# Performance work log

Measured on AMD Instinct MI355X. Metric: run time of the kernel, lower is better.

Reference implementation:

```python
import jax, jax.numpy as jnp
import numpy as np

V, BLOCK, L, H, E, B, T = 1024, 2048, 4, 8, 512, 4, 2048
D = E // H  # head dim = 64

def setup_inputs() -> dict:
    key = jax.random.key(0)
    ks = jax.random.split(key, 8)
    s = 0.02
    return {
        "idx": jax.random.randint(ks[0], (B, T), 0, V),
        "wte": jax.random.normal(ks[1], (V, E), jnp.float32) * s,
        "wpe": jax.random.normal(ks[2], (BLOCK, E), jnp.float32) * s,
        "ln1_w": jnp.ones((L, E), jnp.float32),
        "ln1_b": jnp.zeros((L, E), jnp.float32),
        "attn_w": jax.random.normal(ks[3], (L, 3 * E, E), jnp.float32) * s,
        "attn_b": jnp.zeros((L, 3 * E), jnp.float32),
        "proj_w": jax.random.normal(ks[4], (L, E, E), jnp.float32) * s,
        "proj_b": jnp.zeros((L, E), jnp.float32),
        "ln2_w": jnp.ones((L, E), jnp.float32),
        "ln2_b": jnp.zeros((L, E), jnp.float32),
        "fc_w": jax.random.normal(ks[5], (L, 4 * E, E), jnp.float32) * s,
        "fc_b": jnp.zeros((L, 4 * E), jnp.float32),
        "fc2_w": jax.random.normal(ks[6], (L, E, 4 * E), jnp.float32) * s,
        "fc2_b": jnp.zeros((L, E), jnp.float32),
        "lnf_w": jnp.ones((E,), jnp.float32),
        "lnf_b": jnp.zeros((E,), jnp.float32),
    }

def layer_norm(x, w, b, eps=1e-5):
    mu = jnp.mean(x, axis=-1, keepdims=True)
    var = jnp.var(x, axis=-1, keepdims=True)
    return (x - mu) * jax.lax.rsqrt(var + eps) * w + b

def reference(idx, wte, wpe, ln1_w, ln1_b, attn_w, attn_b, proj_w, proj_b,
              ln2_w, ln2_b, fc_w, fc_b, fc2_w, fc2_b, lnf_w, lnf_b):
    b, t = idx.shape
    x = wte[idx] + wpe[:t]  # (B,T,E)
    causal = jnp.tril(jnp.ones((t, t), bool))
    scale = 1.0 / np.sqrt(D)

    def block(x, p):
        l1w, l1b, aw, ab, pw, pb, l2w, l2b, fw, fb, f2w, f2b = p
        h = layer_norm(x, l1w, l1b)
        qkv = h @ aw.T + ab  # (B,T,3E)
        q, k, v = jnp.split(qkv, 3, axis=-1)
        q = q.reshape(b, t, H, D)
        k = k.reshape(b, t, H, D)
        v = v.reshape(b, t, H, D)
        att = jnp.einsum('bqhd,bkhd->bhqk', q, k) * scale
        att = jnp.where(causal, att, -jnp.inf)
        att = jax.nn.softmax(att, axis=-1)
        y = jnp.einsum('bhqk,bkhd->bqhd', att, v).reshape(b, t, E)
        x = x + y @ pw.T + pb
        h2 = layer_norm(x, l2w, l2b)
        h2 = jax.nn.gelu(h2 @ fw.T + fb, approximate=False)
        x = x + h2 @ f2w.T + f2b
        return x, None

    params = (ln1_w, ln1_b, attn_w, attn_b, proj_w, proj_b,
              ln2_w, ln2_b, fc_w, fc_b, fc2_w, fc2_b)
    x, _ = jax.lax.scan(block, x, params)
    x = layer_norm(x, lnf_w, lnf_b)
    logits = x @ wte.T  # tied lm_head
    return logits
```

## Files before the change

kernel.cpp:

```cpp
#include <hip/hip_runtime.h>
#include <hip/hip_bf16.h>
#include <math.h>

#define B_ 4
#define T_ 2048
#define E_ 512
#define H_ 8
#define D_ 64
#define L_ 4
#define V_ 1024
#define NROWS (B_*T_)
#define KBLK 64
#define KVPAD 72
#define PPAD 72
#define SPLT 16

typedef __hip_bfloat16 bf16;
typedef __attribute__((ext_vector_type(8))) short bf16x8;
typedef __attribute__((ext_vector_type(4))) float f32x4;

__device__ __forceinline__ short f2bf_s(float f) {
    union { bf16 h; short s; } t; t.h = __float2bfloat16(f); return t.s;
}

__device__ __forceinline__ void gload_lds16(const bf16* g, bf16* l) {
    __builtin_amdgcn_global_load_lds((const __attribute__((address_space(1))) void*)g,
                                     (__attribute__((address_space(3))) void*)l, 16, 0, 0);
}

__global__ void f2bf_all(const float* __restrict__ s0, const float* __restrict__ s1,
                         const float* __restrict__ s2, const float* __restrict__ s3,
                         const float* __restrict__ s4, bf16* __restrict__ dst) {
    size_t gi = (size_t)blockIdx.x * 1024 + threadIdx.x * 4;
    const float* src; size_t off;
    if (blockIdx.x < 3072)       { src = s0; off = gi; }
    else if (blockIdx.x < 4096)  { src = s1; off = gi - (size_t)3072 * 1024; }
    else if (blockIdx.x < 8192)  { src = s2; off = gi - (size_t)4096 * 1024; }
    else if (blockIdx.x < 12288) { src = s3; off = gi - (size_t)8192 * 1024; }
    else                         { src = s4; off = gi - (size_t)12288 * 1024; }
    float4 v = *(const float4*)(src + off);
    union { bf16 h[4]; uint2 u; } t;
    t.h[0] = __float2bfloat16(v.x); t.h[1] = __float2bfloat16(v.y);
    t.h[2] = __float2bfloat16(v.z); t.h[3] = __float2bfloat16(v.w);
    *(uint2*)(dst + gi) = t.u;
}

__global__ void embed_kernel(const int* __restrict__ idx, const float* __restrict__ wte,
                             const float* __restrict__ wpe, float* __restrict__ x) {
    int i = (blockIdx.x * blockDim.x + threadIdx.x) * 4;
    int row = i >> 9;
    int e = i & (E_ - 1);
    int t = row & (T_ - 1);
    int id = idx[row];
    float4 a = *(const float4*)(wte + (size_t)id * E_ + e);
    float4 p = *(const float4*)(wpe + (size_t)t * E_ + e);
    a.x += p.x; a.y += p.y; a.z += p.z; a.w += p.w;
    *(float4*)(x + i) = a;
}

__global__ __launch_bounds__(512) void layernorm_kernel(const float* __restrict__ x,
                                 const float* __restrict__ w, const float* __restrict__ b,
                                 bf16* __restrict__ out) {
    int wid = threadIdx.x >> 6, lane = threadIdx.x & 63;
    int row = blockIdx.x * 8 + wid;
    const float* xr = x + (size_t)row * E_ + lane * 8;
    float4 a0 = *(const float4*)xr;
    float4 a1 = *(const float4*)(xr + 4);
    float s = (a0.x + a0.y) + (a0.z + a0.w) + (a1.x + a1.y) + (a1.z + a1.w);
    float q = a0.x*a0.x + a0.y*a0.y + a0.z*a0.z + a0.w*a0.w
            + a1.x*a1.x + a1.y*a1.y + a1.z*a1.z + a1.w*a1.w;
    #pragma unroll
    for (int st = 1; st < 64; st <<= 1) { s += __shfl_xor(s, st); q += __shfl_xor(q, st); }
    float mean = s * (1.0f / E_);
    float var = q * (1.0f / E_) - mean * mean;
    float rstd = rsqrtf(var + 1e-5f);
    float4 w0 = *(const float4*)(w + lane * 8), w1 = *(const float4*)(w + lane * 8 + 4);
    float4 b0 = *(const float4*)(b + lane * 8), b1 = *(const float4*)(b + lane * 8 + 4);
    union { bf16 h[8]; uint4 u; } o;
    o.h[0] = __float2bfloat16((a0.x - mean) * rstd * w0.x + b0.x);
    o.h[1] = __float2bfloat16((a0.y - mean) * rstd * w0.y + b0.y);
    o.h[2] = __float2bfloat16((a0.z - mean) * rstd * w0.z + b0.z);
    o.h[3] = __float2bfloat16((a0.w - mean) * rstd * w0.w + b0.w);
    o.h[4] = __float2bfloat16((a1.x - mean) * rstd * w1.x + b1.x);
    o.h[5] = __float2bfloat16((a1.y - mean) * rstd * w1.y + b1.y);
    o.h[6] = __float2bfloat16((a1.z - mean) * rstd * w1.z + b1.z);
    o.h[7] = __float2bfloat16((a1.w - mean) * rstd * w1.w + b1.w);
    *(uint4*)(out + (size_t)row * E_ + lane * 8) = o.u;
}

template<int ACT, int OMODE, bool BIAS, bool QKV>
__global__ __launch_bounds__(256) void gemm_mfma(const bf16* __restrict__ A, const bf16* __restrict__ W,
        const float* __restrict__ bias, float* __restrict__ Cf, bf16* __restrict__ Cb,
        bf16* __restrict__ Vt, int M, int N, int K) {
    __shared__ __align__(16) bf16 As[128][32];
    __shared__ __align__(16) bf16 Bs[128][32];
    int tid = threadIdx.x;
    int lane = tid & 63, wid = tid >> 6;
    int wm = (wid >> 1) * 64, wn = (wid & 1) * 64;
    int m0 = blockIdx.y * 128, n0 = blockIdx.x * 128;

    int srow = wid * 32 + (lane >> 2);
    int scol = (lane & 3) * 8;
    const bf16* ga = A + (size_t)(m0 + srow) * K + scol;
    const bf16* gb = W + (size_t)(n0 + srow) * K + scol;
    int fr = lane & 15, fk = (lane >> 4) * 8;

    f32x4 acc[4][4];
    #pragma unroll
    for (int i = 0; i < 4; ++i)
        #pragma unroll
        for (int j = 0; j < 4; ++j) acc[i][j] = (f32x4){0.f, 0.f, 0.f, 0.f};

    for (int k0 = 0; k0 < K; k0 += 32) {
        gload_lds16(ga,          &As[wid * 32][0]);
        gload_lds16(ga + 16 * K, &As[wid * 32 + 16][0]);
        gload_lds16(gb,          &Bs[wid * 32][0]);
        gload_lds16(gb + 16 * K, &Bs[wid * 32 + 16][0]);
        ga += 32; gb += 32;
        __syncthreads();
        bf16x8 af[4], bff[4];
        #pragma unroll
        for (int i = 0; i < 4; ++i) af[i]  = *(const bf16x8*)&As[wm + i * 16 + fr][fk];
        #pragma unroll
        for (int j = 0; j < 4; ++j) bff[j] = *(const bf16x8*)&Bs[wn + j * 16 + fr][fk];
        #pragma unroll
        for (int i = 0; i < 4; ++i)
            #pragma unroll
            for (int j = 0; j < 4; ++j)
                acc[i][j] = __builtin_amdgcn_mfma_f32_16x16x32_bf16(af[i], bff[j], acc[i][j], 0, 0, 0);
        __syncthreads();
    }

    int orow = m0 + wm + (lane >> 4) * 4;
    int ocol = n0 + wn + (lane & 15);

    if (QKV && n0 >= 2 * E_) {
        #pragma unroll
        for (int i = 0; i < 4; ++i) {
            int rowb = orow + i * 16;
            int bb = rowb >> 11;
            int t0 = rowb & (T_ - 1);
            #pragma unroll
            for (int j = 0; j < 4; ++j) {
                int col = ocol + j * 16;
                int dg = col - 2 * E_;
                int hh = dg >> 6, dd = dg & 63;
                float bv = BIAS ? bias[col] : 0.0f;
                union { bf16 h[4]; short4 s4; } pk;
                #pragma unroll
                for (int r = 0; r < 4; ++r)
                    pk.h[r] = __float2bfloat16(acc[i][j][r] + bv);
                *(short4*)&Vt[(((size_t)bb * H_ + hh) * D_ + dd) * T_ + t0] = pk.s4;
            }
        }
        return;
    }

    #pragma unroll
    for (int i = 0; i < 4; ++i) {
        #pragma unroll
        for (int j = 0; j < 4; ++j) {
            #pragma unroll
            for (int r = 0; r < 4; ++r) {
                int row = orow + i * 16 + r;
                int col = ocol + j * 16;
                float v = acc[i][j][r];
                if (BIAS) v += bias[col];
                if (ACT == 1) v = 0.5f * v * (1.0f + erff(v * 0.70710678118654752f));
                if (QKV) {
                    if (col < E_) v *= 0.125f;
                    Cb[(size_t)row * (2 * E_) + col] = __float2bfloat16(v);
                } else {
                    size_t off = (size_t)row * N + col;
                    if (OMODE == 0) Cf[off] = v;
                    else if (OMODE == 1) Cb[off] = __float2bfloat16(v);
                    else Cf[off] += v;
                }
            }
        }
    }
}

template<bool DOMASK>
__device__ __forceinline__ void attn_tile(
        const short (&Ks)[KBLK][KVPAD], const short (&VsT)[D_][KVPAD],
        short (*Psw)[PPAD], const bf16x8 (&qf)[2],
        float& m_run, float& l_run, f32x4 (&accO)[4],
        int fr, int fg, int k0, int qrow) {
    f32x4 st[4];
    __builtin_amdgcn_s_setprio(1);
    #pragma unroll
    for (int j = 0; j < 4; ++j) {
        f32x4 a = (f32x4){0.f, 0.f, 0.f, 0.f};
        #pragma unroll
        for (int kk = 0; kk < 2; ++kk) {
            bf16x8 kf = *(const bf16x8*)&Ks[j * 16 + fr][kk * 32 + fg * 8];
            a = __builtin_amdgcn_mfma_f32_16x16x32_bf16(kf, qf[kk], a, 0, 0, 0);
        }
        st[j] = a;
    }
    __builtin_amdgcn_s_setprio(0);
    float mx = -INFINITY;
    #pragma unroll
    for (int j = 0; j < 4; ++j)
        #pragma unroll
        for (int r = 0; r < 4; ++r) {
            if (DOMASK && (k0 + j * 16 + fg * 4 + r > qrow)) st[j][r] = -INFINITY;
            mx = fmaxf(mx, st[j][r]);
        }
    mx = fmaxf(mx, __shfl_xor(mx, 16));
    mx = fmaxf(mx, __shfl_xor(mx, 32));
    if (!__all(mx <= m_run + 8.0f)) {
        float mnew = fmaxf(m_run, mx);
        float corr = __expf(m_run - mnew);
        l_run *= corr;
        #pragma unroll
        for (int r = 0; r < 4; ++r) {
            float cr = __shfl(corr, fg * 4 + r);
            #pragma unroll
            for (int n = 0; n < 4; ++n) accO[n][r] *= cr;
        }
        m_run = mnew;
    }
    float rl = 0.0f;
    #pragma unroll
    for (int j = 0; j < 4; ++j) {
        float p0 = __expf(st[j][0] - m_run), p1 = __expf(st[j][1] - m_run);
        float p2 = __expf(st[j][2] - m_run), p3 = __expf(st[j][3] - m_run);
        rl += (p0 + p1) + (p2 + p3);
        short4 pk;
        pk.x = f2bf_s(p0); pk.y = f2bf_s(p1); pk.z = f2bf_s(p2); pk.w = f2bf_s(p3);
        *(short4*)&Psw[fr][j * 16 + fg * 4] = pk;
    }
    rl += __shfl_xor(rl, 16);
    rl += __shfl_xor(rl, 32);
    l_run += rl;
    __builtin_amdgcn_s_setprio(1);
    bf16x8 pa[2];
    #pragma unroll
    for (int kk = 0; kk < 2; ++kk)
        pa[kk] = *(const bf16x8*)&Psw[fr][kk * 32 + fg * 8];
    #pragma unroll
    for (int n = 0; n < 4; ++n)
        #pragma unroll
        for (int kk = 0; kk < 2; ++kk) {
            bf16x8 vb = *(const bf16x8*)&VsT[n * 16 + fr][kk * 32 + fg * 8];
            accO[n] = __builtin_amdgcn_mfma_f32_16x16x32_bf16(pa[kk], vb, accO[n], 0, 0, 0);
        }
    __builtin_amdgcn_s_setprio(0);
}

__global__ __launch_bounds__(256, 4) void attn_mfma(const bf16* __restrict__ qk,
                                                    const bf16* __restrict__ vt,
                                                    bf16* __restrict__ y,
                                                    bf16* __restrict__ opart,
                                                    float2* __restrict__ mlb) {
    __shared__ __align__(16) short Ks[KBLK][KVPAD];
    __shared__ __align__(16) short VsT[D_][KVPAD];
    __shared__ __align__(16) short Ps[4][16][PPAD];
    const int qi = (gridDim.x - 1) - blockIdx.x;
    const int sp = blockIdx.y >> 3;
    const int h = blockIdx.y & 7, b = blockIdx.z;
    const int nt = qi + 1;
    const bool split_mode = (qi >= SPLT);
    if (!split_mode && sp == 1) return;
    const int t0i = split_mode ? sp * SPLT : 0;
    const int t1i = split_mode ? min(nt, t0i + SPLT) : nt;

    const int q0 = qi * 64;
    const int tid = threadIdx.x;
    const int lane = tid & 63, wid = tid >> 6;
    const int fr = lane & 15, fg = lane >> 4;
    const int qmin = q0 + wid * 16;
    const int qrow = qmin + fr;

    const int sr0 = tid >> 3;
    const int sc = (tid & 7) * 8;
    const bf16* kst = qk + (size_t)(b * T_ + sr0) * (2 * E_) + E_ + h * D_ + sc;
    const bf16* vst = vt + ((size_t)(b * H_ + h) * D_ + sr0) * T_ + sc;

    const bf16* qbase = qk + (size_t)(b * T_ + qrow) * (2 * E_) + h * D_;
    bf16x8 qf[2];
    #pragma unroll
    for (int kk = 0; kk < 2; ++kk)
        qf[kk] = *(const bf16x8*)(qbase + kk * 32 + fg * 8);

    float m_run = -INFINITY, l_run = 0.0f;
    f32x4 accO[4];
    #pragma unroll
    for (int n = 0; n < 4; ++n) accO[n] = (f32x4){0.f, 0.f, 0.f, 0.f};

    {
        const bf16* kp = kst + (size_t)t0i * KBLK * (2 * E_);
        const bf16* vp = vst + t0i * KBLK;
        uint4 k0r = *(const uint4*)kp;
        uint4 k1r = *(const uint4*)(kp + 32 * (2 * E_));
        uint4 v0r = *(const uint4*)vp;
        uint4 v1r = *(const uint4*)(vp + 32 * T_);
        *(uint4*)&Ks[sr0][sc] = k0r;  *(uint4*)&Ks[sr0 + 32][sc] = k1r;
        *(uint4*)&VsT[sr0][sc] = v0r; *(uint4*)&VsT[sr0 + 32][sc] = v1r;
    }
    __syncthreads();

    for (int kt = t0i; kt < t1i; ++kt) {
        const bool have_next = (kt + 1 < t1i);
        uint4 nk0, nk1, nv0, nv1;
        if (have_next) {
            const bf16* kn = kst + (size_t)(kt + 1) * KBLK * (2 * E_);
            const bf16* vn = vst + (kt + 1) * KBLK;
            nk0 = *(const uint4*)kn; nk1 = *(const uint4*)(kn + 32 * (2 * E_));
            nv0 = *(const uint4*)vn; nv1 = *(const uint4*)(vn + 32 * T_);
        }

        if (kt == nt - 1)
            attn_tile<true >(Ks, VsT, Ps[wid], qf, m_run, l_run, accO, fr, fg, kt * KBLK, qrow);
        else
            attn_tile<false>(Ks, VsT, Ps[wid], qf, m_run, l_run, accO, fr, fg, kt * KBLK, qrow);

        __syncthreads();
        if (have_next) {
            *(uint4*)&Ks[sr0][sc] = nk0;  *(uint4*)&Ks[sr0 + 32][sc] = nk1;
            *(uint4*)&VsT[sr0][sc] = nv0; *(uint4*)&VsT[sr0 + 32][sc] = nv1;
            __syncthreads();
        }
    }

    if (split_mode) {
        size_t rbase = (size_t)sp * 32768 + (size_t)b * 8192 + (size_t)h * 1024 + (qmin - 1024);
        if (lane < 16) mlb[rbase + lane] = make_float2(m_run, l_run);
        #pragma unroll
        for (int r = 0; r < 4; ++r) {
            #pragma unroll
            for (int n = 0; n < 4; ++n)
                opart[(rbase + fg * 4 + r) * D_ + n * 16 + fr] = __float2bfloat16(accO[n][r]);
        }
    } else {
        float linv = 1.0f / l_run;
        #pragma unroll
        for (int r = 0; r < 4; ++r) {
            float lr = __shfl(linv, fg * 4 + r);
            int gq = qmin + fg * 4 + r;
            #pragma unroll
            for (int n = 0; n < 4; ++n)
                y[(size_t)(b * T_ + gq) * E_ + h * D_ + n * 16 + fr] =
                    __float2bfloat16(accO[n][r] * lr);
        }
    }
}

__global__ __launch_bounds__(512) void attn_combine(const bf16* __restrict__ opart,
        const float2* __restrict__ mlb, bf16* __restrict__ y) {
    int lane = threadIdx.x & 63, wid = threadIdx.x >> 6;
    int row = blockIdx.x * 8 + wid;
    int b = row >> 13, h = (row >> 10) & 7, trel = row & 1023;
    float2 s0 = mlb[row];
    float2 s1 = mlb[32768 + row];
    float mm = fmaxf(s0.x, s1.x);
    float w0 = __expf(s0.x - mm), w1 = __expf(s1.x - mm);
    float l = w0 * s0.y + w1 * s1.y;
    float o = w0 * __bfloat162float(opart[(size_t)row * D_ + lane])
            + w1 * __bfloat162float(opart[((size_t)32768 + row) * D_ + lane]);
    y[(size_t)(b * T_ + 1024 + trel) * E_ + h * D_ + lane] = __float2bfloat16(o / l);
}

extern "C" void kernel_launch(void* const* d_in, const int* in_sizes, int n_in,
                              void* d_out, int out_size, void* d_ws, size_t ws_size,
                              hipStream_t stream) {
    const int*   idx    = (const int*)d_in[0];
    const float* wte    = (const float*)d_in[1];
    const float* wpe    = (const float*)d_in[2];
    const float* ln1_w  = (const float*)d_in[3];
    const float* ln1_b  = (const float*)d_in[4];
    const float* attn_w = (const float*)d_in[5];
    const float* attn_b = (const float*)d_in[6];
    const float* proj_w = (const float*)d_in[7];
    const float* proj_b = (const float*)d_in[8];
    const float* ln2_w  = (const float*)d_in[9];
    const float* ln2_b  = (const float*)d_in[10];
    const float* fc_w   = (const float*)d_in[11];
    const float* fc_b   = (const float*)d_in[12];
    const float* fc2_w  = (const float*)d_in[13];
    const float* fc2_b  = (const float*)d_in[14];
    const float* lnf_w  = (const float*)d_in[15];
    const float* lnf_b  = (const float*)d_in[16];
    float* out = (float*)d_out;

    float* x   = (float*)d_ws;
    bf16* hbf  = (bf16*)(x + (size_t)NROWS * E_);
    bf16* big  = hbf + (size_t)NROWS * E_;
    bf16* qkb  = big;
    bf16* vtb  = big + (size_t)NROWS * 2 * E_;
    bf16* opart = big + (size_t)NROWS * 3 * E_;
    bf16* wb   = big + (size_t)NROWS * 4 * E_;
    bf16* attn_wb = wb;
    bf16* proj_wb = attn_wb + (size_t)L_ * 3 * E_ * E_;
    bf16* fc_wb   = proj_wb + (size_t)L_ * E_ * E_;
    bf16* fc2_wb  = fc_wb   + (size_t)L_ * 4 * E_ * E_;
    bf16* wte_b   = fc2_wb  + (size_t)L_ * E_ * 4 * E_;
    float2* mlb   = (float2*)(wte_b + (size_t)V_ * E_);

    f2bf_all<<<12800, 256, 0, stream>>>(attn_w, proj_w, fc_w, fc2_w, wte, wb);
    embed_kernel<<<NROWS * E_ / 1024, 256, 0, stream>>>(idx, wte, wpe, x);

    for (int l = 0; l < L_; ++l) {
        layernorm_kernel<<<NROWS / 8, 512, 0, stream>>>(x, ln1_w + l * E_, ln1_b + l * E_, hbf);
        gemm_mfma<0, 1, true, true><<<dim3(3 * E_ / 128, NROWS / 128), 256, 0, stream>>>(
            hbf, attn_wb + (size_t)l * 3 * E_ * E_, attn_b + l * 3 * E_, nullptr, qkb, vtb,
            NROWS, 3 * E_, E_);
        attn_mfma<<<dim3(T_ / 64, H_ * 2, B_), 256, 0, stream>>>(qkb, vtb, hbf, opart, mlb);
        attn_combine<<<32768 / 8, 512, 0, stream>>>(opart, mlb, hbf);
        gemm_mfma<0, 2, true, false><<<dim3(E_ / 128, NROWS / 128), 256, 0, stream>>>(
            hbf, proj_wb + (size_t)l * E_ * E_, proj_b + l * E_, x, nullptr, nullptr,
            NROWS, E_, E_);
        layernorm_kernel<<<NROWS / 8, 512, 0, stream>>>(x, ln2_w + l * E_, ln2_b + l * E_, hbf);
        gemm_mfma<1, 1, true, false><<<dim3(4 * E_ / 128, NROWS / 128), 256, 0, stream>>>(
            hbf, fc_wb + (size_t)l * 4 * E_ * E_, fc_b + l * 4 * E_, nullptr, big, nullptr,
            NROWS, 4 * E_, E_);
        gemm_mfma<0, 2, true, false><<<dim3(E_ / 128, NROWS / 128), 256, 0, stream>>>(
            big, fc2_wb + (size_t)l * E_ * 4 * E_, fc2_b + l * E_, x, nullptr, nullptr,
            NROWS, E_, 4 * E_);
    }
    layernorm_kernel<<<NROWS / 8, 512, 0, stream>>>(x, lnf_w, lnf_b, hbf);
    gemm_mfma<0, 0, false, false><<<dim3(V_ / 128, NROWS / 128), 256, 0, stream>>>(
        hbf, wte_b, nullptr, out, nullptr, nullptr, NROWS, V_, E_);
}
```

Baseline: 1.008 ms.

## Deepen GEMM K-step to 64 and pass attention P via lane shuffles

The GEMM now loads two 32-wide K slices per iteration into doubled LDS buffers, which halves the number of barrier pairs per tile. In attention, the bf16 probabilities are packed in registers and redistributed across lanes with shuffles into the MFMA A-operand layout, so the per-wave LDS P scratchpad goes away. Occupancy hint for attention is raised to 8 blocks per CU. The tradeoffs are more shuffle instructions, more GEMM LDS use, and register pressure under the tighter launch bound.

```diff
diff --git a/kernel.cpp b/kernel.cpp
--- a/kernel.cpp
+++ b/kernel.cpp
@@ -12,7 +12,6 @@
 #define NROWS (B_*T_)
 #define KBLK 64
 #define KVPAD 72
-#define PPAD 72
 #define SPLT 16
 
 typedef __hip_bfloat16 bf16;
@@ -21,6 +20,10 @@
 
 __device__ __forceinline__ short f2bf_s(float f) {
     union { bf16 h; short s; } t; t.h = __float2bfloat16(f); return t.s;
+}
+__device__ __forceinline__ unsigned int pack2bf(float a, float b) {
+    return (unsigned int)(unsigned short)f2bf_s(a) |
+           ((unsigned int)(unsigned short)f2bf_s(b) << 16);
 }
 
 __device__ __forceinline__ void gload_lds16(const bf16* g, bf16* l) {
@@ -92,8 +95,8 @@
 __global__ __launch_bounds__(256) void gemm_mfma(const bf16* __restrict__ A, const bf16* __restrict__ W,
         const float* __restrict__ bias, float* __restrict__ Cf, bf16* __restrict__ Cb,
         bf16* __restrict__ Vt, int M, int N, int K) {
-    __shared__ __align__(16) bf16 As[128][32];
-    __shared__ __align__(16) bf16 Bs[128][32];
+    __shared__ __align__(16) bf16 As[2][128][32];
+    __shared__ __align__(16) bf16 Bs[2][128][32];
     int tid = threadIdx.x;
     int lane = tid & 63, wid = tid >> 6;
     int wm = (wid >> 1) * 64, wn = (wid & 1) * 64;
@@ -111,23 +114,30 @@
         #pragma unroll
         for (int j = 0; j < 4; ++j) acc[i][j] = (f32x4){0.f, 0.f, 0.f, 0.f};
 
-    for (int k0 = 0; k0 < K; k0 += 32) {
-        gload_lds16(ga,          &As[wid * 32][0]);
-        gload_lds16(ga + 16 * K, &As[wid * 32 + 16][0]);
-        gload_lds16(gb,          &Bs[wid * 32][0]);
-        gload_lds16(gb + 16 * K, &Bs[wid * 32 + 16][0]);
-        ga += 32; gb += 32;
+    for (int k0 = 0; k0 < K; k0 += 64) {
+        gload_lds16(ga,               &As[0][wid * 32][0]);
+        gload_lds16(ga + 16 * K,      &As[0][wid * 32 + 16][0]);
+        gload_lds16(ga + 32,          &As[1][wid * 32][0]);
+        gload_lds16(ga + 16 * K + 32, &As[1][wid * 32 + 16][0]);
+        gload_lds16(gb,               &Bs[0][wid * 32][0]);
+        gload_lds16(gb + 16 * K,      &Bs[0][wid * 32 + 16][0]);
+        gload_lds16(gb + 32,          &Bs[1][wid * 32][0]);
+        gload_lds16(gb + 16 * K + 32, &Bs[1][wid * 32 + 16][0]);
+        ga += 64; gb += 64;
         __syncthreads();
-        bf16x8 af[4], bff[4];
-        #pragma unroll
-        for (int i = 0; i < 4; ++i) af[i]  = *(const bf16x8*)&As[wm + i * 16 + fr][fk];
-        #pragma unroll
-        for (int j = 0; j < 4; ++j) bff[j] = *(const bf16x8*)&Bs[wn + j * 16 + fr][fk];
-        #pragma unroll
-        for (int i = 0; i < 4; ++i)
-            #pragma unroll
-            for (int j = 0; j < 4; ++j)
-                acc[i][j] = __builtin_amdgcn_mfma_f32_16x16x32_bf16(af[i], bff[j], acc[i][j], 0, 0, 0);
+        #pragma unroll
+        for (int s = 0; s < 2; ++s) {
+            bf16x8 af[4], bff[4];
+            #pragma unroll
+            for (int i = 0; i < 4; ++i) af[i]  = *(const bf16x8*)&As[s][wm + i * 16 + fr][fk];
+            #pragma unroll
+            for (int j = 0; j < 4; ++j) bff[j] = *(const bf16x8*)&Bs[s][wn + j * 16 + fr][fk];
+            #pragma unroll
+            for (int i = 0; i < 4; ++i)
+                #pragma unroll
+                for (int j = 0; j < 4; ++j)
+                    acc[i][j] = __builtin_amdgcn_mfma_f32_16x16x32_bf16(af[i], bff[j], acc[i][j], 0, 0, 0);
+        }
         __syncthreads();
     }
 
@@ -184,7 +194,7 @@
 template<bool DOMASK>
 __device__ __forceinline__ void attn_tile(
         const short (&Ks)[KBLK][KVPAD], const short (&VsT)[D_][KVPAD],
-        short (*Psw)[PPAD], const bf16x8 (&qf)[2],
+        const bf16x8 (&qf)[2],
         float& m_run, float& l_run, f32x4 (&accO)[4],
         int fr, int fg, int k0, int qrow) {
     f32x4 st[4];
@@ -222,24 +232,37 @@
         }
         m_run = mnew;
     }
+    unsigned int dw[4][2];
     float rl = 0.0f;
     #pragma unroll
     for (int j = 0; j < 4; ++j) {
         float p0 = __expf(st[j][0] - m_run), p1 = __expf(st[j][1] - m_run);
         float p2 = __expf(st[j][2] - m_run), p3 = __expf(st[j][3] - m_run);
         rl += (p0 + p1) + (p2 + p3);
-        short4 pk;
-        pk.x = f2bf_s(p0); pk.y = f2bf_s(p1); pk.z = f2bf_s(p2); pk.w = f2bf_s(p3);
-        *(short4*)&Psw[fr][j * 16 + fg * 4] = pk;
+        dw[j][0] = pack2bf(p0, p1);
+        dw[j][1] = pack2bf(p2, p3);
     }
     rl += __shfl_xor(rl, 16);
     rl += __shfl_xor(rl, 32);
     l_run += rl;
+    const int laneA = ((fg & 1) << 5) + fr;
+    const int laneB = laneA + 16;
+    const bool selhi = (fg & 2) != 0;
+    bf16x8 pa[2];
+    #pragma unroll
+    for (int kk = 0; kk < 2; ++kk) {
+        unsigned int a0 = __shfl(dw[2 * kk][0], laneA), a1 = __shfl(dw[2 * kk + 1][0], laneA);
+        unsigned int b0 = __shfl(dw[2 * kk][1], laneA), b1 = __shfl(dw[2 * kk + 1][1], laneA);
+        unsigned int c0 = __shfl(dw[2 * kk][0], laneB), c1 = __shfl(dw[2 * kk + 1][0], laneB);
+        unsigned int d0 = __shfl(dw[2 * kk][1], laneB), d1 = __shfl(dw[2 * kk + 1][1], laneB);
+        union { unsigned int u[4]; bf16x8 v; } t;
+        t.u[0] = selhi ? a1 : a0;
+        t.u[1] = selhi ? b1 : b0;
+        t.u[2] = selhi ? c1 : c0;
+        t.u[3] = selhi ? d1 : d0;
+        pa[kk] = t.v;
+    }
     __builtin_amdgcn_s_setprio(1);
-    bf16x8 pa[2];
-    #pragma unroll
-    for (int kk = 0; kk < 2; ++kk)
-        pa[kk] = *(const bf16x8*)&Psw[fr][kk * 32 + fg * 8];
     #pragma unroll
     for (int n = 0; n < 4; ++n)
         #pragma unroll
@@ -250,14 +273,13 @@
     __builtin_amdgcn_s_setprio(0);
 }
 
-__global__ __launch_bounds__(256, 4) void attn_mfma(const bf16* __restrict__ qk,
+__global__ __launch_bounds__(256, 8) void attn_mfma(const bf16* __restrict__ qk,
                                                     const bf16* __restrict__ vt,
                                                     bf16* __restrict__ y,
                                                     bf16* __restrict__ opart,
                                                     float2* __restrict__ mlb) {
     __shared__ __align__(16) short Ks[KBLK][KVPAD];
     __shared__ __align__(16) short VsT[D_][KVPAD];
-    __shared__ __align__(16) short Ps[4][16][PPAD];
     const int qi = (gridDim.x - 1) - blockIdx.x;
     const int sp = blockIdx.y >> 3;
     const int h = blockIdx.y & 7, b = blockIdx.z;
@@ -313,9 +335,9 @@
         }
 
         if (kt == nt - 1)
-            attn_tile<true >(Ks, VsT, Ps[wid], qf, m_run, l_run, accO, fr, fg, kt * KBLK, qrow);
+            attn_tile<true >(Ks, VsT, qf, m_run, l_run, accO, fr, fg, kt * KBLK, qrow);
         else
-            attn_tile<false>(Ks, VsT, Ps[wid], qf, m_run, l_run, accO, fr, fg, kt * KBLK, qrow);
+            attn_tile<false>(Ks, VsT, qf, m_run, l_run, accO, fr, fg, kt * KBLK, qrow);
 
         __syncthreads();
         if (have_next) {
```

New measurement: 1.678 ms. +66.4%, slower.
